# Performance work log

Measured on AMD Instinct MI355X. Metric: run time of the kernel, lower is better.

The kernel has to match this reference:

```python
import jax, jax.numpy as jnp
import numpy as np
from jax import lax

B, N, S, K, C, OUT = 8, 4096, 1024, 24, 64, 128
IN = 2 * C + 3  # 131: grouped(C+3) concat anchor feature(C)
EPS_BN = 1e-5


def _bn_params(key, c):
    k1, k2, k3, k4 = jax.random.split(key, 4)
    gamma = jax.random.uniform(k1, (c,), minval=0.5, maxval=1.5)
    beta = jax.random.normal(k2, (c,)) * 0.1
    mean = jax.random.normal(k3, (c,)) * 0.1
    var = jax.random.uniform(k4, (c,), minval=0.5, maxval=1.5)
    return jnp.stack([gamma, beta, mean, var])  # [4,c]


def setup_inputs() -> dict:
    key = jax.random.key(0)
    ks = jax.random.split(key, 20)
    w = lambda k, shp: jax.random.normal(k, shp) * 0.05
    inp = {
        "xyz": jax.random.normal(ks[0], (B, N, 3)),
        "points": jax.random.normal(ks[1], (B, N, C)),
        "affine_alpha": jnp.ones((1, 1, 1, C + 3)),
        "affine_beta": jnp.zeros((1, 1, 1, C + 3)),
        "transfer_w": w(ks[2], (OUT, IN)),
        "transfer_b": jnp.zeros((OUT,)),
        "transfer_bn": _bn_params(ks[3], OUT),
        "pre_w1": w(ks[4], (2, OUT, OUT)),
        "pre_b1": jnp.zeros((2, OUT)),
        "pre_bn1": jnp.stack([_bn_params(ks[5], OUT), _bn_params(ks[6], OUT)]),
        "pre_w2": w(ks[7], (2, OUT, OUT)),
        "pre_b2": jnp.zeros((2, OUT)),
        "pre_bn2": jnp.stack([_bn_params(ks[8], OUT), _bn_params(ks[9], OUT)]),
        "pos_w1": w(ks[10], (2, OUT, OUT)),
        "pos_b1": jnp.zeros((2, OUT)),
        "pos_bn1": jnp.stack([_bn_params(ks[11], OUT), _bn_params(ks[12], OUT)]),
        "pos_w2": w(ks[13], (2, OUT, OUT)),
        "pos_b2": jnp.zeros((2, OUT)),
        "pos_bn2": jnp.stack([_bn_params(ks[14], OUT), _bn_params(ks[15], OUT)]),
    }
    return inp


def _gather(x, idx):
    # x: [B,N,D], idx: [B,...] -> [B,...,D]
    return jax.vmap(lambda a, i: a[i])(x, idx)


def _sqdist(a, b):
    # a: [B,S,3], b: [B,N,3] -> [B,S,N]
    return (jnp.sum(a * a, -1)[:, :, None] + jnp.sum(b * b, -1)[:, None, :]
            - 2.0 * jnp.einsum('bsd,bnd->bsn', a, b))


def _fps(xyz, s):
    # furthest point sampling, starts at index 0 (matches CUDA pointnet2 impl)
    b, n, _ = xyz.shape
    def step(carry, _):
        dist, last = carry
        p = jnp.take_along_axis(xyz, last[:, None, None], axis=1)  # [B,1,3]
        d = jnp.sum((xyz - p) ** 2, -1)
        dist = jnp.minimum(dist, d)
        nxt = jnp.argmax(dist, axis=-1).astype(jnp.int32)
        return (dist, nxt), nxt
    init = (jnp.full((b, n), 1e10, xyz.dtype), jnp.zeros((b,), jnp.int32))
    _, idxs = lax.scan(step, init, None, length=s - 1)  # [S-1,B]
    return jnp.concatenate([jnp.zeros((1, b), jnp.int32), idxs], 0).T  # [B,S]


def _conv_bn(x, w, b, bn, act=True):
    # 1x1 Conv1d + BatchNorm (eval mode) + optional ReLU. x: [M,Cin,L]
    y = jnp.einsum('oc,mcl->mol', w, x) + b[None, :, None]
    g, be, mu, var = bn[0], bn[1], bn[2], bn[3]
    y = (y - mu[None, :, None]) * (g[None, :, None] / jnp.sqrt(var[None, :, None] + EPS_BN)) + be[None, :, None]
    return jax.nn.relu(y) if act else y


def _res_block(x, w1, b1, bn1, w2, b2, bn2):
    y = _conv_bn(x, w1, b1, bn1, act=True)
    y = _conv_bn(y, w2, b2, bn2, act=False)
    return jax.nn.relu(y + x)


def reference(xyz, points, affine_alpha, affine_beta,
              transfer_w, transfer_b, transfer_bn,
              pre_w1, pre_b1, pre_bn1, pre_w2, pre_b2, pre_bn2,
              pos_w1, pos_b1, pos_bn1, pos_w2, pos_b2, pos_bn2):
    b, n, _ = xyz.shape
    # ---- LocalGrouper ----
    fps_idx = _fps(xyz, S)                      # [B,S]
    new_xyz = _gather(xyz, fps_idx)             # [B,S,3]
    new_points = _gather(points, fps_idx)       # [B,S,C]
    d = _sqdist(new_xyz, xyz)                   # [B,S,N]
    _, idx = lax.top_k(-d, K)                   # k nearest -> [B,S,K]
    grouped_xyz = _gather(xyz, idx)             # [B,S,K,3]
    grouped_points = _gather(points, idx)       # [B,S,K,C]
    grouped = jnp.concatenate([grouped_points, grouped_xyz], -1)  # [B,S,K,C+3]
    # anchor normalize
    mean = jnp.concatenate([new_points, new_xyz], -1)[:, :, None, :]
    diff = grouped - mean
    std = jnp.std(diff.reshape(b, -1), axis=-1, ddof=1)[:, None, None, None]
    grouped = affine_alpha * (diff / (std + 1e-5)) + affine_beta
    anchor = jnp.broadcast_to(new_points[:, :, None, :], (b, S, K, C))
    feats = jnp.concatenate([grouped, anchor], -1)  # [B,S,K,2C+3]
    # ---- PreExtraction ----
    x = feats.transpose(0, 1, 3, 2).reshape(b * S, IN, K)  # [B*S,131,K]
    x = _conv_bn(x, transfer_w, transfer_b, transfer_bn, act=True)
    for i in range(2):
        x = _res_block(x, pre_w1[i], pre_b1[i], pre_bn1[i], pre_w2[i], pre_b2[i], pre_bn2[i])
    x = jnp.max(x, axis=-1)                     # adaptive max pool over K
    x = x.reshape(b, S, OUT).transpose(0, 2, 1)  # [B,OUT,S]
    # ---- PosExtraction ----
    for i in range(2):
        x = _res_block(x, pos_w1[i], pos_b1[i], pos_bn1[i], pos_w2[i], pos_b2[i], pos_bn2[i])
    return x  # [B,128,1024]
```

## Files before the change

### kernel.cpp

```cpp
#include <hip/hip_runtime.h>
#include <hip/hip_bf16.h>
#include <stdint.h>
#include <math.h>

#define DEVINL static __device__ __forceinline__

static constexpr int BB = 8, NN = 4096, SS = 1024, KK = 24, CC = 64;
static constexpr int INCH = 131, OUTCH = 128;

typedef __attribute__((ext_vector_type(8))) short short8v;
typedef __attribute__((ext_vector_type(4))) float f32x4;
typedef __attribute__((ext_vector_type(2))) float f32x2;

#define MFMA16(a, b, c) __builtin_amdgcn_mfma_f32_16x16x32_bf16(a, b, c, 0, 0, 0)

DEVINL unsigned short bfhi(float v) {
  return (unsigned short)(__float_as_uint(v) >> 16);
}
DEVINL float bfhif(float v) {
  return __uint_as_float(__float_as_uint(v) & 0xFFFF0000u);
}
DEVINL unsigned short bflo(float v) {
  float r = __fsub_rn(v, bfhif(v));
  return (unsigned short)(__float_as_uint(r) >> 16);
}

__global__ __launch_bounds__(256) void k_prep_xyz(
    const float* __restrict__ xyz,
    float* __restrict__ xs, float* __restrict__ ys,
    float* __restrict__ zs, float* __restrict__ sb) {
  int e = blockIdx.x * 256 + threadIdx.x;
  if (e >= BB * NN) return;
  float x = xyz[e * 3 + 0];
  float y = xyz[e * 3 + 1];
  float z = xyz[e * 3 + 2];
  xs[e] = x; ys[e] = y; zs[e] = z;
  sb[e] = __fadd_rn(__fadd_rn(__fmul_rn(x, x), __fmul_rn(y, y)), __fmul_rn(z, z));
}

__global__ __launch_bounds__(256) void k_prep_w(
    const float* __restrict__ tw,
    const float* __restrict__ pw1, const float* __restrict__ pw2,
    const float* __restrict__ qw1, const float* __restrict__ qw2,
    const float* __restrict__ tb,  const float* __restrict__ tbn,
    const float* __restrict__ pb1, const float* __restrict__ pbn1,
    const float* __restrict__ pb2, const float* __restrict__ pbn2,
    const float* __restrict__ qb1, const float* __restrict__ qbn1,
    const float* __restrict__ qb2, const float* __restrict__ qbn2,
    float* __restrict__ wt_sq, float* __restrict__ bnsb,
    unsigned short* __restrict__ wfhi, unsigned short* __restrict__ wflo) {
  int e = blockIdx.x * 256 + threadIdx.x;
  const int NSQ = 8 * 128 * 128;
  const int NBN = 9 * 128;
  const int NFR = 168 * 64;
  if (e < NSQ) {
    int layer = e >> 14, m = e & 16383;
    int ci = m >> 7, co = m & 127;
    const float* src;
    switch (layer) {
      case 0: src = pw1;         break;
      case 1: src = pw2;         break;
      case 2: src = pw1 + 16384; break;
      case 3: src = pw2 + 16384; break;
      case 4: src = qw1;         break;
      case 5: src = qw2;         break;
      case 6: src = qw1 + 16384; break;
      default: src = qw2 + 16384; break;
    }
    wt_sq[layer * 16384 + ci * 128 + co] = src[co * 128 + ci];
  } else if (e < NSQ + NBN) {
    int r = e - NSQ;
    int L = r >> 7, co = r & 127;
    const float *bn, *bc;
    switch (L) {
      case 0: bn = tbn;        bc = tb;        break;
      case 1: bn = pbn1;       bc = pb1;       break;
      case 2: bn = pbn2;       bc = pb2;       break;
      case 3: bn = pbn1 + 512; bc = pb1 + 128; break;
      case 4: bn = pbn2 + 512; bc = pb2 + 128; break;
      case 5: bn = qbn1;       bc = qb1;       break;
      case 6: bn = qbn2;       bc = qb2;       break;
      case 7: bn = qbn1 + 512; bc = qb1 + 128; break;
      default: bn = qbn2 + 512; bc = qb2 + 128; break;
    }
    float g  = bn[co];
    float be = bn[128 + co];
    float mu = bn[256 + co];
    float va = bn[384 + co];
    float bcv = bc[co];
    float sc = g / sqrtf(va + 1e-5f);
    float bi = (bcv - mu) * sc + be;
    bnsb[L * 256 + co] = sc;
    bnsb[L * 256 + 128 + co] = bi;
  } else if (e < NSQ + NBN + NFR) {
    int r = e - (NSQ + NBN);
    int T = r >> 6, lane = r & 63;
    int L, ks, mt;
    if (T < 40) { L = 0; ks = T >> 3; mt = T & 7; }
    else { int r2 = T - 40; L = 1 + (r2 >> 5); int r3 = r2 & 31; ks = r3 >> 3; mt = r3 & 7; }
    const float* src;
    int K, stride;
    switch (L) {
      case 0:  src = tw;          K = 131; stride = 131; break;
      case 1:  src = pw1;         K = 128; stride = 128; break;
      case 2:  src = pw2;         K = 128; stride = 128; break;
      case 3:  src = pw1 + 16384; K = 128; stride = 128; break;
      default: src = pw2 + 16384; K = 128; stride = 128; break;
    }
    int m = lane & 15, kb = lane >> 4;
    int co = mt * 16 + m;
    int base = (T * 64 + lane) * 8;
#pragma unroll
    for (int j = 0; j < 8; j++) {
      int ci = ks * 32 + kb * 8 + j;
      float w = (ci < K) ? src[co * stride + ci] : 0.f;
      wfhi[base + j] = bfhi(w);
      wflo[base + j] = bflo(w);
    }
  }
}

DEVINL float wave_max_f32_l63(float x) {
#define STEPF(C)                                                                \
  {                                                                             \
    int o = __builtin_amdgcn_update_dpp(0xff800000, __float_as_int(x), C, 0xf, 0xf, false); \
    x = fmaxf(x, __int_as_float(o));                                            \
  }
  STEPF(0x111) STEPF(0x112) STEPF(0x114) STEPF(0x118) STEPF(0x142) STEPF(0x143)
#undef STEPF
  return x;
}

__global__ __launch_bounds__(256, 1) void k_fps(
    const float* __restrict__ xs, const float* __restrict__ ys,
    const float* __restrict__ zs, const float* __restrict__ sb,
    const float* __restrict__ points,
    float* __restrict__ nxyz, float* __restrict__ sa, float* __restrict__ newp) {
  __shared__ float lxl[NN], lyl[NN], lzl[NN];
  __shared__ unsigned long long pk[2][4];
  __shared__ int fpsl[SS];
  const int b = blockIdx.x, t = threadIdx.x;
  const int wid = t >> 6, lane = t & 63;
  const float* bx = xs + b * NN;
  const float* by = ys + b * NN;
  const float* bz = zs + b * NN;
  f32x2 rx[8], ry[8], rz[8], d[8];
  const int n0 = t * 16;
#pragma unroll
  for (int j = 0; j < 8; j++) {
    int n = n0 + 2 * j;
    rx[j].x = bx[n]; rx[j].y = bx[n + 1];
    ry[j].x = by[n]; ry[j].y = by[n + 1];
    rz[j].x = bz[n]; rz[j].y = bz[n + 1];
    lxl[n] = rx[j].x; lxl[n + 1] = rx[j].y;
    lyl[n] = ry[j].x; lyl[n + 1] = ry[j].y;
    lzl[n] = rz[j].x; lzl[n + 1] = rz[j].y;
    d[j].x = 1e10f; d[j].y = 1e10f;
  }
  __syncthreads();
  float px = lxl[0], py = lyl[0], pz = lzl[0];
  if (t == 0) fpsl[0] = 0;
#pragma unroll 1
  for (int i = 1; i < SS; i++) {
    float bestval = -1.f;
    int bestn = 0;
    f32x2 px2, py2, pz2;
    px2.x = px; px2.y = px;
    py2.x = py; py2.y = py;
    pz2.x = pz; pz2.y = pz;
#pragma unroll
    for (int j = 0; j < 8; j++) {
      f32x2 dd;
      {
#pragma clang fp contract(off)
        f32x2 dx = rx[j] - px2;
        f32x2 dy = ry[j] - py2;
        f32x2 dz = rz[j] - pz2;
        dd = (dx * dx + dy * dy) + dz * dz;
      }
      float nd0 = fminf(d[j].x, dd.x);
      float nd1 = fminf(d[j].y, dd.y);
      d[j].x = nd0; d[j].y = nd1;
      if (nd0 > bestval) { bestval = nd0; bestn = n0 + 2 * j; }
      if (nd1 > bestval) { bestval = nd1; bestn = n0 + 2 * j + 1; }
    }
    float wmax = __int_as_float(
        __builtin_amdgcn_readlane(__float_as_int(wave_max_f32_l63(bestval)), 63));
    unsigned long long el = __ballot(bestval == wmax);
    int fl = (int)__ffsll(el) - 1;
    int wn = __builtin_amdgcn_readlane(bestn, fl);
    if (lane == 0)
      pk[i & 1][wid] = ((unsigned long long)__float_as_uint(wmax) << 32) |
                       (unsigned)(NN - 1 - wn);
    __syncthreads();
    const unsigned long long* P = pk[i & 1];
    unsigned long long k0 = P[0], k1 = P[1], k2 = P[2], k3 = P[3];
    unsigned long long m01 = k1 > k0 ? k1 : k0;
    unsigned long long m23 = k3 > k2 ? k3 : k2;
    unsigned long long g = m23 > m01 ? m23 : m01;
    int n = NN - 1 - (int)(unsigned)g;
    px = lxl[n]; py = lyl[n]; pz = lzl[n];
    if (t == 0) fpsl[i] = n;
  }
  __syncthreads();
  for (int s = t; s < SS; s += 256) {
    int row = fpsl[s];
    nxyz[(b * SS + s) * 3 + 0] = lxl[row];
    nxyz[(b * SS + s) * 3 + 1] = lyl[row];
    nxyz[(b * SS + s) * 3 + 2] = lzl[row];
    sa[b * SS + s] = sb[b * NN + row];
  }
  for (int e = t; e < SS * CC; e += 256) {
    int s = e >> 6, c = e & 63;
    int row = fpsl[s];
    newp[(b * SS + s) * CC + c] = points[(b * NN + row) * CC + c];
  }
}

__global__ __launch_bounds__(256, 2) void k_knn(
    const float* __restrict__ xs, const float* __restrict__ ys,
    const float* __restrict__ zs,
    const float* __restrict__ nxyz, const float* __restrict__ sa,
    const float* __restrict__ points, const float* __restrict__ newp,
    int* __restrict__ knn, double* __restrict__ spart) {
  __shared__ float lx[NN], ly[NN], lz[NN];
  __shared__ int selk[4][KK];
  const int blk = blockIdx.x, t = threadIdx.x, wid = t >> 6, lane = t & 63;
  const int b = blk >> 8;
  for (int e = t; e < NN; e += 256) {
    lx[e] = xs[b * NN + e]; ly[e] = ys[b * NN + e]; lz[e] = zs[b * NN + e];
  }
  __syncthreads();
  const int q = blk * 4 + wid;
  float qx = nxyz[q * 3 + 0], qy = nxyz[q * 3 + 1], qz = nxyz[q * 3 + 2];
  float qa = sa[q];
  unsigned keys[64];
#pragma unroll
  for (int j = 0; j < 64; j++) {
    int n = j * 64 + lane;
    float x = lx[n], y = ly[n], z = lz[n];
    float sbn = __fadd_rn(__fadd_rn(__fmul_rn(x, x), __fmul_rn(y, y)), __fmul_rn(z, z));
    float dot = __fadd_rn(__fadd_rn(__fmul_rn(qx, x), __fmul_rn(qy, y)), __fmul_rn(qz, z));
    float dd = __fsub_rn(__fadd_rn(qa, sbn), __fmul_rn(2.0f, dot));
    unsigned u = __float_as_uint(dd);
    u ^= (0x80000000u | (unsigned)((int)u >> 31));
    keys[j] = u;
  }
#pragma unroll 1
  for (int r = 0; r < KK; r++) {
    unsigned bv = keys[0];
    int bj = 0;
#pragma unroll
    for (int j = 1; j < 64; j++) {
      if (keys[j] < bv) { bv = keys[j]; bj = j; }
    }
    unsigned long long gk = ((unsigned long long)bv << 32) | (unsigned)(bj * 64 + lane);
#pragma unroll
    for (int m = 1; m < 64; m <<= 1) {
      unsigned long long o = __shfl_xor(gk, m);
      gk = o < gk ? o : gk;
    }
    int n = (int)(unsigned)gk;
    if (lane == 0) { knn[q * KK + r] = n; selk[wid][r] = n; }
    if (lane == (n & 63)) {
      int jj = n >> 6;
#pragma unroll
      for (int j = 0; j < 64; j++)
        if (j == jj) keys[j] = 0xFFFFFFFFu;
    }
  }
  double s1 = 0.0, s2 = 0.0;
#pragma unroll 1
  for (int i = 0; i < 26; i++) {
    int e = lane + 64 * i;
    if (e < KK * 67) {
      int k = e / 67, c = e - k * 67;
      int n = selk[wid][k];
      float g, mm;
      if (c < CC) {
        g = points[(b * NN + n) * CC + c];
        mm = newp[q * CC + c];
      } else {
        int cc = c - CC;
        g = cc == 0 ? lx[n] : (cc == 1 ? ly[n] : lz[n]);
        mm = nxyz[q * 3 + cc];
      }
      float v = __fsub_rn(g, mm);
      s1 += (double)v;
      s2 += (double)v * (double)v;
    }
  }
#pragma unroll
  for (int m = 1; m < 64; m <<= 1) {
    s1 += __shfl_xor(s1, m);
    s2 += __shfl_xor(s2, m);
  }
  if (lane == 0) { spart[q * 2 + 0] = s1; spart[q * 2 + 1] = s2; }
}

__global__ __launch_bounds__(256) void k_stdfin(
    const double* __restrict__ spart, float* __restrict__ stdp) {
  __shared__ double a1[256], a2[256];
  const int b = blockIdx.x, t = threadIdx.x;
  double s1 = 0.0, s2 = 0.0;
  for (int i = t; i < SS; i += 256) {
    s1 += spart[(b * SS + i) * 2 + 0];
    s2 += spart[(b * SS + i) * 2 + 1];
  }
  a1[t] = s1; a2[t] = s2;
  __syncthreads();
  for (int w = 128; w > 0; w >>= 1) {
    if (t < w) { a1[t] += a1[t + w]; a2[t] += a2[t + w]; }
    __syncthreads();
  }
  if (t == 0) {
    const double n = (double)SS * KK * 67;
    double m = a1[0] / n;
    double var = (a2[0] - a1[0] * m) / (n - 1.0);
    if (var < 0.0) var = 0.0;
    float stdf = (float)sqrt(var);
    stdp[b] = stdf + 1e-5f;
  }
}

static constexpr int BST = 168;
static constexpr int XST = 132;

__global__ __launch_bounds__(256, 4) void k_pre(
    const float* __restrict__ points,
    const float* __restrict__ alpha, const float* __restrict__ beta,
    const float* __restrict__ xs, const float* __restrict__ ys, const float* __restrict__ zs,
    const float* __restrict__ nxyz, const float* __restrict__ newp,
    const float* __restrict__ stdp, const int* __restrict__ knn,
    const unsigned short* __restrict__ wfhi, const unsigned short* __restrict__ wflo,
    const float* __restrict__ bnsb, float* __restrict__ pre_out) {
  __shared__ unsigned short Bhi[32 * BST];
  __shared__ unsigned short Blo[32 * BST];
  __shared__ float Xres[32 * XST];
  __shared__ int kn[KK];
  __shared__ float npl[CC], nxl[3], al[67], bt[67];
  __shared__ float stds;
  const int q = blockIdx.x, b = q >> 10, t = threadIdx.x;
  for (int e = t; e < 32 * BST; e += 256) { Bhi[e] = 0; Blo[e] = 0; }
  if (t < KK) kn[t] = knn[q * KK + t];
  if (t < 67) { al[t] = alpha[t]; bt[t] = beta[t]; }
  if (t < CC) npl[t] = newp[q * CC + t];
  if (t < 3) nxl[t] = nxyz[q * 3 + t];
  if (t == 0) stds = stdp[b];
  __syncthreads();
  for (int e = t; e < KK * 67; e += 256) {
    int k = e / 67, c = e - k * 67;
    int n = kn[k];
    float g, mm;
    if (c < CC) {
      g = points[(b * NN + n) * CC + c];
      mm = npl[c];
    } else {
      int cc = c - CC;
      g = cc == 0 ? xs[b * NN + n] : (cc == 1 ? ys[b * NN + n] : zs[b * NN + n]);
      mm = nxl[cc];
    }
    float v = __fsub_rn(g, mm);
    float tt = __fdiv_rn(v, stds);
    float val = __fadd_rn(__fmul_rn(al[c], tt), bt[c]);
    Bhi[k * BST + c] = bfhi(val);
    Blo[k * BST + c] = bflo(val);
  }
  for (int e = t; e < CC * KK; e += 256) {
    int c = e / KK, k = e - c * KK;
    float val = npl[c];
    Bhi[k * BST + 67 + c] = bfhi(val);
    Blo[k * BST + 67 + c] = bflo(val);
  }
  __syncthreads();

  const int wv = t >> 6, lane = t & 63;
  const int g4 = lane >> 4;
  const int l15 = lane & 15;
  const int mt0 = wv * 2;

#pragma unroll
  for (int L = 0; L < 5; ++L) {
    const int nks = (L == 0) ? 5 : 4;
    const int wtb = (L == 0) ? 0 : (8 + 32 * L);
    const bool addres = (L == 2) || (L == 4);
    const bool wres = (L == 0) || (L == 2);
    const bool pool = (L == 4);
    f32x4 acc00 = {0.f, 0.f, 0.f, 0.f}, acc01 = {0.f, 0.f, 0.f, 0.f};
    f32x4 acc10 = {0.f, 0.f, 0.f, 0.f}, acc11 = {0.f, 0.f, 0.f, 0.f};
#pragma unroll
    for (int ks = 0; ks < nks; ++ks) {
      const int tb = (wtb + ks * 8 + mt0) * 64 + lane;
      short8v wh0 = *(const short8v*)(wfhi + tb * 8);
      short8v wh1 = *(const short8v*)(wfhi + (tb + 64) * 8);
      short8v wl0 = *(const short8v*)(wflo + tb * 8);
      short8v wl1 = *(const short8v*)(wflo + (tb + 64) * 8);
      const int bo = l15 * BST + ks * 32 + g4 * 8;
      short8v bh0 = *(const short8v*)&Bhi[bo];
      short8v bh1 = *(const short8v*)&Bhi[bo + 16 * BST];
      short8v bl0 = *(const short8v*)&Blo[bo];
      short8v bl1 = *(const short8v*)&Blo[bo + 16 * BST];
      acc00 = MFMA16(wh0, bh0, acc00);
      acc00 = MFMA16(wl0, bh0, acc00);
      acc00 = MFMA16(wh0, bl0, acc00);
      acc01 = MFMA16(wh0, bh1, acc01);
      acc01 = MFMA16(wl0, bh1, acc01);
      acc01 = MFMA16(wh0, bl1, acc01);
      acc10 = MFMA16(wh1, bh0, acc10);
      acc10 = MFMA16(wl1, bh0, acc10);
      acc10 = MFMA16(wh1, bl0, acc10);
      acc11 = MFMA16(wh1, bh1, acc11);
      acc11 = MFMA16(wl1, bh1, acc11);
      acc11 = MFMA16(wh1, bl1, acc11);
    }
    __syncthreads();
    float mx0[4] = {0.f, 0.f, 0.f, 0.f};
    float mx1[4] = {0.f, 0.f, 0.f, 0.f};
    auto ep = [&](const f32x4& a, int mt_i, int nt, float* mxr) {
      const int co0 = (mt0 + mt_i) * 16 + g4 * 4;
      const int kp = nt * 16 + l15;
      const bool valid = kp < KK;
      f32x4 scv = *(const f32x4*)(bnsb + L * 256 + co0);
      f32x4 biv = *(const f32x4*)(bnsb + L * 256 + 128 + co0);
      float y[4];
#pragma unroll
      for (int r = 0; r < 4; r++) y[r] = fmaf(a[r], scv[r], biv[r]);
      if (addres && valid) {
        f32x4 xr = *(const f32x4*)&Xres[kp * XST + co0];
#pragma unroll
        for (int r = 0; r < 4; r++) y[r] += xr[r];
      }
#pragma unroll
      for (int r = 0; r < 4; r++) y[r] = fmaxf(y[r], 0.f);
      if (wres && valid) {
        f32x4 o = {y[0], y[1], y[2], y[3]};
        *(f32x4*)&Xres[kp * XST + co0] = o;
      }
      if (!pool) {
        if (valid) {
          unsigned b0 = __float_as_uint(y[0]), b1 = __float_as_uint(y[1]);
          unsigned b2 = __float_as_uint(y[2]), b3 = __float_as_uint(y[3]);
          unsigned h01 = (b0 >> 16) | (b1 & 0xFFFF0000u);
          unsigned h23 = (b2 >> 16) | (b3 & 0xFFFF0000u);
          *(uint2*)&Bhi[kp * BST + co0] = make_uint2(h01, h23);
          float r0 = __fsub_rn(y[0], __uint_as_float(b0 & 0xFFFF0000u));
          float r1 = __fsub_rn(y[1], __uint_as_float(b1 & 0xFFFF0000u));
          float r2 = __fsub_rn(y[2], __uint_as_float(b2 & 0xFFFF0000u));
          float r3 = __fsub_rn(y[3], __uint_as_float(b3 & 0xFFFF0000u));
          unsigned l01 = (__float_as_uint(r0) >> 16) | (__float_as_uint(r1) & 0xFFFF0000u);
          unsigned l23 = (__float_as_uint(r2) >> 16) | (__float_as_uint(r3) & 0xFFFF0000u);
          *(uint2*)&Blo[kp * BST + co0] = make_uint2(l01, l23);
        }
      } else {
#pragma unroll
        for (int r = 0; r < 4; r++) {
          float v = valid ? y[r] : 0.f;
          mxr[r] = fmaxf(mxr[r], v);
        }
      }
    };
    ep(acc00, 0, 0, mx0);
    ep(acc01, 0, 1, mx0);
    ep(acc10, 1, 0, mx1);
    ep(acc11, 1, 1, mx1);
    if (!pool) {
      __syncthreads();
    } else {
#pragma unroll
      for (int dstep = 1; dstep < 16; dstep <<= 1) {
#pragma unroll
        for (int r = 0; r < 4; r++) {
          mx0[r] = fmaxf(mx0[r], __shfl_xor(mx0[r], dstep));
          mx1[r] = fmaxf(mx1[r], __shfl_xor(mx1[r], dstep));
        }
      }
      if (l15 == 0) {
        f32x4 o0 = {mx0[0], mx0[1], mx0[2], mx0[3]};
        f32x4 o1 = {mx1[0], mx1[1], mx1[2], mx1[3]};
        *(f32x4*)&pre_out[q * 128 + mt0 * 16 + g4 * 4] = o0;
        *(f32x4*)&pre_out[q * 128 + (mt0 + 1) * 16 + g4 * 4] = o1;
      }
    }
  }
}

__global__ __launch_bounds__(256, 2) void k_pos(
    const float* __restrict__ pre_out, const float* __restrict__ wt_sq,
    const float* __restrict__ bnsb, float* __restrict__ out) {
  __shared__ float X[128][68];
  __shared__ float Y[128][68];
  const int blk = blockIdx.x, t = threadIdx.x;
  const int b = blk >> 4, s0 = (blk & 15) << 6;
  for (int e = t; e < 128 * 64; e += 256) {
    int sl = e >> 7, c = e & 127;
    X[c][sl] = pre_out[(b * SS + s0 + sl) * 128 + c];
  }
  __syncthreads();
  const int co0 = (t >> 3) << 2, p0 = (t & 7) << 3;
  float acc[4][8];
  auto conv = [&](const float (*IN)[68], const float* wt) {
#pragma unroll
    for (int i = 0; i < 4; i++)
#pragma unroll
      for (int j = 0; j < 8; j++) acc[i][j] = 0.f;
#pragma unroll 2
    for (int ci = 0; ci < 128; ci++) {
      float4 w = *(const float4*)(wt + ci * 128 + co0);
      float4 r0 = *(const float4*)&IN[ci][p0];
      float4 r1 = *(const float4*)&IN[ci][p0 + 4];
      float a[8] = {r0.x, r0.y, r0.z, r0.w, r1.x, r1.y, r1.z, r1.w};
#pragma unroll
      for (int j = 0; j < 8; j++) {
        acc[0][j] = fmaf(w.x, a[j], acc[0][j]);
        acc[1][j] = fmaf(w.y, a[j], acc[1][j]);
        acc[2][j] = fmaf(w.z, a[j], acc[2][j]);
        acc[3][j] = fmaf(w.w, a[j], acc[3][j]);
      }
    }
  };
  conv(X, wt_sq + 4 * 16384);
  {
    const float* bn = bnsb + 5 * 256;
#pragma unroll
    for (int i = 0; i < 4; i++) {
      float sc = bn[co0 + i], bi = bn[128 + co0 + i];
#pragma unroll
      for (int j = 0; j < 8; j++)
        Y[co0 + i][p0 + j] = fmaxf(fmaf(acc[i][j], sc, bi), 0.f);
    }
  }
  __syncthreads();
  conv(Y, wt_sq + 5 * 16384);
  {
    const float* bn = bnsb + 6 * 256;
#pragma unroll
    for (int i = 0; i < 4; i++) {
      float sc = bn[co0 + i], bi = bn[128 + co0 + i];
#pragma unroll
      for (int j = 0; j < 8; j++)
        X[co0 + i][p0 + j] =
            fmaxf(fmaf(acc[i][j], sc, bi) + X[co0 + i][p0 + j], 0.f);
    }
  }
  __syncthreads();
  conv(X, wt_sq + 6 * 16384);
  {
    const float* bn = bnsb + 7 * 256;
#pragma unroll
    for (int i = 0; i < 4; i++) {
      float sc = bn[co0 + i], bi = bn[128 + co0 + i];
#pragma unroll
      for (int j = 0; j < 8; j++)
        Y[co0 + i][p0 + j] = fmaxf(fmaf(acc[i][j], sc, bi), 0.f);
    }
  }
  __syncthreads();
  conv(Y, wt_sq + 7 * 16384);
  {
    const float* bn = bnsb + 8 * 256;
#pragma unroll
    for (int i = 0; i < 4; i++) {
      float sc = bn[co0 + i], bi = bn[128 + co0 + i];
      float4 o0, o1;
      float v;
      v = fmaxf(fmaf(acc[i][0], sc, bi) + X[co0 + i][p0 + 0], 0.f); o0.x = v;
      v = fmaxf(fmaf(acc[i][1], sc, bi) + X[co0 + i][p0 + 1], 0.f); o0.y = v;
      v = fmaxf(fmaf(acc[i][2], sc, bi) + X[co0 + i][p0 + 2], 0.f); o0.z = v;
      v = fmaxf(fmaf(acc[i][3], sc, bi) + X[co0 + i][p0 + 3], 0.f); o0.w = v;
      v = fmaxf(fmaf(acc[i][4], sc, bi) + X[co0 + i][p0 + 4], 0.f); o1.x = v;
      v = fmaxf(fmaf(acc[i][5], sc, bi) + X[co0 + i][p0 + 5], 0.f); o1.y = v;
      v = fmaxf(fmaf(acc[i][6], sc, bi) + X[co0 + i][p0 + 6], 0.f); o1.z = v;
      v = fmaxf(fmaf(acc[i][7], sc, bi) + X[co0 + i][p0 + 7], 0.f); o1.w = v;
      float* op = &out[(size_t)(b * 128 + co0 + i) * SS + s0 + p0];
      *(float4*)op = o0;
      *(float4*)(op + 4) = o1;
    }
  }
}

extern "C" void kernel_launch(void* const* d_in, const int* in_sizes, int n_in,
                              void* d_out, int out_size, void* d_ws, size_t ws_size,
                              hipStream_t stream) {
  (void)in_sizes; (void)n_in; (void)out_size; (void)ws_size;
  const float* xyz    = (const float*)d_in[0];
  const float* points = (const float*)d_in[1];
  const float* alpha  = (const float*)d_in[2];
  const float* beta   = (const float*)d_in[3];
  const float* tw     = (const float*)d_in[4];
  const float* tb     = (const float*)d_in[5];
  const float* tbn    = (const float*)d_in[6];
  const float* pw1    = (const float*)d_in[7];
  const float* pb1    = (const float*)d_in[8];
  const float* pbn1   = (const float*)d_in[9];
  const float* pw2    = (const float*)d_in[10];
  const float* pb2    = (const float*)d_in[11];
  const float* pbn2   = (const float*)d_in[12];
  const float* qw1    = (const float*)d_in[13];
  const float* qb1    = (const float*)d_in[14];
  const float* qbn1   = (const float*)d_in[15];
  const float* qw2    = (const float*)d_in[16];
  const float* qb2    = (const float*)d_in[17];
  const float* qbn2   = (const float*)d_in[18];

  char* ws = (char*)d_ws;
  size_t off = 0;
  auto alloc = [&](size_t bytes) -> char* {
    char* p = ws + off;
    off += (bytes + 255) & ~(size_t)255;
    return p;
  };
  float*  xs    = (float*)alloc(BB * NN * 4);
  float*  ys    = (float*)alloc(BB * NN * 4);
  float*  zs    = (float*)alloc(BB * NN * 4);
  float*  sb    = (float*)alloc(BB * NN * 4);
  float*  wt_sq = (float*)alloc(8 * 16384 * 4);
  float*  bnsb  = (float*)alloc(9 * 256 * 4);
  unsigned short* wfhi = (unsigned short*)alloc(168 * 512 * 2);
  unsigned short* wflo = (unsigned short*)alloc(168 * 512 * 2);
  float*  nxyz  = (float*)alloc(BB * SS * 3 * 4);
  float*  sa    = (float*)alloc(BB * SS * 4);
  float*  newp  = (float*)alloc(BB * SS * CC * 4);
  int*    knn   = (int*)alloc(BB * SS * KK * 4);
  double* spart = (double*)alloc(BB * SS * 2 * 8);
  float*  stdp  = (float*)alloc(256);
  float*  preo  = (float*)alloc((size_t)BB * SS * 128 * 4);
  float*  out   = (float*)d_out;

  const int prep_n = 8 * 128 * 128 + 9 * 128 + 168 * 64;
  hipLaunchKernelGGL(k_prep_xyz, dim3((BB * NN + 255) / 256), dim3(256), 0, stream,
                     xyz, xs, ys, zs, sb);
  hipLaunchKernelGGL(k_prep_w, dim3((prep_n + 255) / 256), dim3(256), 0, stream,
                     tw, pw1, pw2, qw1, qw2, tb, tbn, pb1, pbn1, pb2, pbn2,
                     qb1, qbn1, qb2, qbn2, wt_sq, bnsb, wfhi, wflo);
  hipLaunchKernelGGL(k_fps, dim3(BB), dim3(256), 0, stream,
                     xs, ys, zs, sb, points, nxyz, sa, newp);
  hipLaunchKernelGGL(k_knn, dim3(BB * SS / 4), dim3(256), 0, stream,
                     xs, ys, zs, nxyz, sa, points, newp, knn, spart);
  hipLaunchKernelGGL(k_stdfin, dim3(BB), dim3(256), 0, stream, spart, stdp);
  hipLaunchKernelGGL(k_pre, dim3(BB * SS), dim3(256), 0, stream,
                     points, alpha, beta, xs, ys, zs, nxyz, newp, stdp, knn,
                     wfhi, wflo, bnsb, preo);
  hipLaunchKernelGGL(k_pos, dim3(BB * SS / 64), dim3(256), 0, stream,
                     preo, wt_sq, bnsb, out);
}
```

Measured before the change: 1.036 ms.

## Process two query groups per k_pre block and use DPP wave-min in kNN

k_pre now handles two sampled centroids per block, so each block keeps two sets of shared-memory activation tiles and reuses every loaded weight fragment for both groups' MFMAs. This halves global weight traffic per centroid and halves the block count. The cost is twice the LDS footprint, more accumulator registers and lower launch bounds occupancy (4 to 2). Separately, the kNN argmin over a wave replaces a 64-bit shuffle-xor butterfly with two 32-bit DPP min reductions plus readlane.

```diff
diff --git a/kernel.cpp b/kernel.cpp
--- a/kernel.cpp
+++ b/kernel.cpp
@@ -131,6 +131,28 @@
   return x;
 }
 
+DEVINL unsigned wave_min_u32_l63(unsigned x) {
+#define STEPU(C)                                                                \
+  {                                                                             \
+    unsigned o = (unsigned)__builtin_amdgcn_update_dpp(-1, (int)x, C, 0xf, 0xf, false); \
+    x = o < x ? o : x;                                                          \
+  }
+  STEPU(0x111) STEPU(0x112) STEPU(0x114) STEPU(0x118) STEPU(0x142) STEPU(0x143)
+#undef STEPU
+  return x;
+}
+
+DEVINL int wave_min_i32_l63(int x) {
+#define STEPI(C)                                                                \
+  {                                                                             \
+    int o = __builtin_amdgcn_update_dpp(0x7fffffff, x, C, 0xf, 0xf, false);     \
+    x = o < x ? o : x;                                                          \
+  }
+  STEPI(0x111) STEPI(0x112) STEPI(0x114) STEPI(0x118) STEPI(0x142) STEPI(0x143)
+#undef STEPI
+  return x;
+}
+
 __global__ __launch_bounds__(256, 1) void k_fps(
     const float* __restrict__ xs, const float* __restrict__ ys,
     const float* __restrict__ zs, const float* __restrict__ sb,
@@ -254,13 +276,10 @@
     for (int j = 1; j < 64; j++) {
       if (keys[j] < bv) { bv = keys[j]; bj = j; }
     }
-    unsigned long long gk = ((unsigned long long)bv << 32) | (unsigned)(bj * 64 + lane);
-#pragma unroll
-    for (int m = 1; m < 64; m <<= 1) {
-      unsigned long long o = __shfl_xor(gk, m);
-      gk = o < gk ? o : gk;
-    }
-    int n = (int)(unsigned)gk;
+    unsigned wmin = (unsigned)__builtin_amdgcn_readlane(
+        (int)wave_min_u32_l63(bv), 63);
+    int en = (bv == wmin) ? (bj * 64 + lane) : 0x7FFFFFFF;
+    int n = __builtin_amdgcn_readlane(wave_min_i32_l63(en), 63);
     if (lane == 0) { knn[q * KK + r] = n; selk[wid][r] = n; }
     if (lane == (n & 63)) {
       int jj = n >> 6;
@@ -326,7 +345,7 @@
 static constexpr int BST = 168;
 static constexpr int XST = 132;
 
-__global__ __launch_bounds__(256, 4) void k_pre(
+__global__ __launch_bounds__(256, 2) void k_pre(
     const float* __restrict__ points,
     const float* __restrict__ alpha, const float* __restrict__ beta,
     const float* __restrict__ xs, const float* __restrict__ ys, const float* __restrict__ zs,
@@ -334,43 +353,49 @@
     const float* __restrict__ stdp, const int* __restrict__ knn,
     const unsigned short* __restrict__ wfhi, const unsigned short* __restrict__ wflo,
     const float* __restrict__ bnsb, float* __restrict__ pre_out) {
-  __shared__ unsigned short Bhi[32 * BST];
-  __shared__ unsigned short Blo[32 * BST];
-  __shared__ float Xres[32 * XST];
-  __shared__ int kn[KK];
-  __shared__ float npl[CC], nxl[3], al[67], bt[67];
+  __shared__ unsigned short Bhi[2][32 * BST];
+  __shared__ unsigned short Blo[2][32 * BST];
+  __shared__ float Xres[2][32 * XST];
+  __shared__ int kn[2][KK];
+  __shared__ float npl[2][CC], nxl[2][3], al[67], bt[67];
   __shared__ float stds;
-  const int q = blockIdx.x, b = q >> 10, t = threadIdx.x;
-  for (int e = t; e < 32 * BST; e += 256) { Bhi[e] = 0; Blo[e] = 0; }
-  if (t < KK) kn[t] = knn[q * KK + t];
+  const int q0 = blockIdx.x * 2, b = q0 >> 10, t = threadIdx.x;
+  for (int e = t; e < 32 * BST; e += 256) {
+    Bhi[0][e] = 0; Blo[0][e] = 0; Bhi[1][e] = 0; Blo[1][e] = 0;
+  }
+  if (t < 2 * KK) kn[t / KK][t % KK] = knn[(q0 + t / KK) * KK + (t % KK)];
   if (t < 67) { al[t] = alpha[t]; bt[t] = beta[t]; }
-  if (t < CC) npl[t] = newp[q * CC + t];
-  if (t < 3) nxl[t] = nxyz[q * 3 + t];
+  if (t < 2 * CC) { int s = t >> 6, c = t & 63; npl[s][c] = newp[(q0 + s) * CC + c]; }
+  if (t < 6) { int s = t / 3, c = t % 3; nxl[s][c] = nxyz[(q0 + s) * 3 + c]; }
   if (t == 0) stds = stdp[b];
   __syncthreads();
-  for (int e = t; e < KK * 67; e += 256) {
-    int k = e / 67, c = e - k * 67;
-    int n = kn[k];
+  for (int e = t; e < 2 * KK * 67; e += 256) {
+    int s = e / (KK * 67);
+    int r = e - s * (KK * 67);
+    int k = r / 67, c = r - k * 67;
+    int n = kn[s][k];
     float g, mm;
     if (c < CC) {
       g = points[(b * NN + n) * CC + c];
-      mm = npl[c];
+      mm = npl[s][c];
     } else {
       int cc = c - CC;
       g = cc == 0 ? xs[b * NN + n] : (cc == 1 ? ys[b * NN + n] : zs[b * NN + n]);
-      mm = nxl[cc];
+      mm = nxl[s][cc];
     }
     float v = __fsub_rn(g, mm);
     float tt = __fdiv_rn(v, stds);
     float val = __fadd_rn(__fmul_rn(al[c], tt), bt[c]);
-    Bhi[k * BST + c] = bfhi(val);
-    Blo[k * BST + c] = bflo(val);
-  }
-  for (int e = t; e < CC * KK; e += 256) {
-    int c = e / KK, k = e - c * KK;
-    float val = npl[c];
-    Bhi[k * BST + 67 + c] = bfhi(val);
-    Blo[k * BST + 67 + c] = bflo(val);
+    Bhi[s][k * BST + c] = bfhi(val);
+    Blo[s][k * BST + c] = bflo(val);
+  }
+  for (int e = t; e < 2 * CC * KK; e += 256) {
+    int s = e / (CC * KK);
+    int r = e - s * (CC * KK);
+    int c = r / KK, k = r - c * KK;
+    float val = npl[s][c];
+    Bhi[s][k * BST + 67 + c] = bfhi(val);
+    Blo[s][k * BST + 67 + c] = bflo(val);
   }
   __syncthreads();
 
@@ -386,8 +411,8 @@
     const bool addres = (L == 2) || (L == 4);
     const bool wres = (L == 0) || (L == 2);
     const bool pool = (L == 4);
-    f32x4 acc00 = {0.f, 0.f, 0.f, 0.f}, acc01 = {0.f, 0.f, 0.f, 0.f};
-    f32x4 acc10 = {0.f, 0.f, 0.f, 0.f}, acc11 = {0.f, 0.f, 0.f, 0.f};
+    f32x4 aA00 = {0,0,0,0}, aA01 = {0,0,0,0}, aA10 = {0,0,0,0}, aA11 = {0,0,0,0};
+    f32x4 aB00 = {0,0,0,0}, aB01 = {0,0,0,0}, aB10 = {0,0,0,0}, aB11 = {0,0,0,0};
 #pragma unroll
     for (int ks = 0; ks < nks; ++ks) {
       const int tb = (wtb + ks * 8 + mt0) * 64 + lane;
@@ -396,27 +421,47 @@
       short8v wl0 = *(const short8v*)(wflo + tb * 8);
       short8v wl1 = *(const short8v*)(wflo + (tb + 64) * 8);
       const int bo = l15 * BST + ks * 32 + g4 * 8;
-      short8v bh0 = *(const short8v*)&Bhi[bo];
-      short8v bh1 = *(const short8v*)&Bhi[bo + 16 * BST];
-      short8v bl0 = *(const short8v*)&Blo[bo];
-      short8v bl1 = *(const short8v*)&Blo[bo + 16 * BST];
-      acc00 = MFMA16(wh0, bh0, acc00);
-      acc00 = MFMA16(wl0, bh0, acc00);
-      acc00 = MFMA16(wh0, bl0, acc00);
-      acc01 = MFMA16(wh0, bh1, acc01);
-      acc01 = MFMA16(wl0, bh1, acc01);
-      acc01 = MFMA16(wh0, bl1, acc01);
-      acc10 = MFMA16(wh1, bh0, acc10);
-      acc10 = MFMA16(wl1, bh0, acc10);
-      acc10 = MFMA16(wh1, bl0, acc10);
-      acc11 = MFMA16(wh1, bh1, acc11);
-      acc11 = MFMA16(wl1, bh1, acc11);
-      acc11 = MFMA16(wh1, bl1, acc11);
+      {
+        short8v bh0 = *(const short8v*)&Bhi[0][bo];
+        short8v bh1 = *(const short8v*)&Bhi[0][bo + 16 * BST];
+        short8v bl0 = *(const short8v*)&Blo[0][bo];
+        short8v bl1 = *(const short8v*)&Blo[0][bo + 16 * BST];
+        aA00 = MFMA16(wh0, bh0, aA00);
+        aA00 = MFMA16(wl0, bh0, aA00);
+        aA00 = MFMA16(wh0, bl0, aA00);
+        aA01 = MFMA16(wh0, bh1, aA01);
+        aA01 = MFMA16(wl0, bh1, aA01);
+        aA01 = MFMA16(wh0, bl1, aA01);
+        aA10 = MFMA16(wh1, bh0, aA10);
+        aA10 = MFMA16(wl1, bh0, aA10);
+        aA10 = MFMA16(wh1, bl0, aA10);
+        aA11 = MFMA16(wh1, bh1, aA11);
+        aA11 = MFMA16(wl1, bh1, aA11);
+        aA11 = MFMA16(wh1, bl1, aA11);
+      }
+      {
+        short8v bh0 = *(const short8v*)&Bhi[1][bo];
+        short8v bh1 = *(const short8v*)&Bhi[1][bo + 16 * BST];
+        short8v bl0 = *(const short8v*)&Blo[1][bo];
+        short8v bl1 = *(const short8v*)&Blo[1][bo + 16 * BST];
+        aB00 = MFMA16(wh0, bh0, aB00);
+        aB00 = MFMA16(wl0, bh0, aB00);
+        aB00 = MFMA16(wh0, bl0, aB00);
+        aB01 = MFMA16(wh0, bh1, aB01);
+        aB01 = MFMA16(wl0, bh1, aB01);
+        aB01 = MFMA16(wh0, bl1, aB01);
+        aB10 = MFMA16(wh1, bh0, aB10);
+        aB10 = MFMA16(wl1, bh0, aB10);
+        aB10 = MFMA16(wh1, bl0, aB10);
+        aB11 = MFMA16(wh1, bh1, aB11);
+        aB11 = MFMA16(wl1, bh1, aB11);
+        aB11 = MFMA16(wh1, bl1, aB11);
+      }
     }
     __syncthreads();
-    float mx0[4] = {0.f, 0.f, 0.f, 0.f};
-    float mx1[4] = {0.f, 0.f, 0.f, 0.f};
-    auto ep = [&](const f32x4& a, int mt_i, int nt, float* mxr) {
+    float mxA0[4] = {0,0,0,0}, mxA1[4] = {0,0,0,0};
+    float mxB0[4] = {0,0,0,0}, mxB1[4] = {0,0,0,0};
+    auto ep = [&](const f32x4& a, int s, int mt_i, int nt, float* mxr) {
       const int co0 = (mt0 + mt_i) * 16 + g4 * 4;
       const int kp = nt * 16 + l15;
       const bool valid = kp < KK;
@@ -426,7 +471,7 @@
 #pragma unroll
       for (int r = 0; r < 4; r++) y[r] = fmaf(a[r], scv[r], biv[r]);
       if (addres && valid) {
-        f32x4 xr = *(const f32x4*)&Xres[kp * XST + co0];
+        f32x4 xr = *(const f32x4*)&Xres[s][kp * XST + co0];
 #pragma unroll
         for (int r = 0; r < 4; r++) y[r] += xr[r];
       }
@@ -434,7 +479,7 @@
       for (int r = 0; r < 4; r++) y[r] = fmaxf(y[r], 0.f);
       if (wres && valid) {
         f32x4 o = {y[0], y[1], y[2], y[3]};
-        *(f32x4*)&Xres[kp * XST + co0] = o;
+        *(f32x4*)&Xres[s][kp * XST + co0] = o;
       }
       if (!pool) {
         if (valid) {
@@ -442,14 +487,14 @@
           unsigned b2 = __float_as_uint(y[2]), b3 = __float_as_uint(y[3]);
           unsigned h01 = (b0 >> 16) | (b1 & 0xFFFF0000u);
           unsigned h23 = (b2 >> 16) | (b3 & 0xFFFF0000u);
-          *(uint2*)&Bhi[kp * BST + co0] = make_uint2(h01, h23);
+          *(uint2*)&Bhi[s][kp * BST + co0] = make_uint2(h01, h23);
           float r0 = __fsub_rn(y[0], __uint_as_float(b0 & 0xFFFF0000u));
           float r1 = __fsub_rn(y[1], __uint_as_float(b1 & 0xFFFF0000u));
           float r2 = __fsub_rn(y[2], __uint_as_float(b2 & 0xFFFF0000u));
           float r3 = __fsub_rn(y[3], __uint_as_float(b3 & 0xFFFF0000u));
           unsigned l01 = (__float_as_uint(r0) >> 16) | (__float_as_uint(r1) & 0xFFFF0000u);
           unsigned l23 = (__float_as_uint(r2) >> 16) | (__float_as_uint(r3) & 0xFFFF0000u);
-          *(uint2*)&Blo[kp * BST + co0] = make_uint2(l01, l23);
+          *(uint2*)&Blo[s][kp * BST + co0] = make_uint2(l01, l23);
         }
       } else {
 #pragma unroll
@@ -459,10 +504,14 @@
         }
       }
     };
-    ep(acc00, 0, 0, mx0);
-    ep(acc01, 0, 1, mx0);
-    ep(acc10, 1, 0, mx1);
-    ep(acc11, 1, 1, mx1);
+    ep(aA00, 0, 0, 0, mxA0);
+    ep(aA01, 0, 0, 1, mxA0);
+    ep(aA10, 0, 1, 0, mxA1);
+    ep(aA11, 0, 1, 1, mxA1);
+    ep(aB00, 1, 0, 0, mxB0);
+    ep(aB01, 1, 0, 1, mxB0);
+    ep(aB10, 1, 1, 0, mxB1);
+    ep(aB11, 1, 1, 1, mxB1);
     if (!pool) {
       __syncthreads();
     } else {
@@ -470,15 +519,21 @@
       for (int dstep = 1; dstep < 16; dstep <<= 1) {
 #pragma unroll
         for (int r = 0; r < 4; r++) {
-          mx0[r] = fmaxf(mx0[r], __shfl_xor(mx0[r], dstep));
-          mx1[r] = fmaxf(mx1[r], __shfl_xor(mx1[r], dstep));
+          mxA0[r] = fmaxf(mxA0[r], __shfl_xor(mxA0[r], dstep));
+          mxA1[r] = fmaxf(mxA1[r], __shfl_xor(mxA1[r], dstep));
+          mxB0[r] = fmaxf(mxB0[r], __shfl_xor(mxB0[r], dstep));
+          mxB1[r] = fmaxf(mxB1[r], __shfl_xor(mxB1[r], dstep));
         }
       }
       if (l15 == 0) {
-        f32x4 o0 = {mx0[0], mx0[1], mx0[2], mx0[3]};
-        f32x4 o1 = {mx1[0], mx1[1], mx1[2], mx1[3]};
-        *(f32x4*)&pre_out[q * 128 + mt0 * 16 + g4 * 4] = o0;
-        *(f32x4*)&pre_out[q * 128 + (mt0 + 1) * 16 + g4 * 4] = o1;
+        f32x4 oA0 = {mxA0[0], mxA0[1], mxA0[2], mxA0[3]};
+        f32x4 oA1 = {mxA1[0], mxA1[1], mxA1[2], mxA1[3]};
+        f32x4 oB0 = {mxB0[0], mxB0[1], mxB0[2], mxB0[3]};
+        f32x4 oB1 = {mxB1[0], mxB1[1], mxB1[2], mxB1[3]};
+        *(f32x4*)&pre_out[q0 * 128 + mt0 * 16 + g4 * 4] = oA0;
+        *(f32x4*)&pre_out[q0 * 128 + (mt0 + 1) * 16 + g4 * 4] = oA1;
+        *(f32x4*)&pre_out[(q0 + 1) * 128 + mt0 * 16 + g4 * 4] = oB0;
+        *(f32x4*)&pre_out[(q0 + 1) * 128 + (mt0 + 1) * 16 + g4 * 4] = oB1;
       }
     }
   }
@@ -637,7 +692,7 @@
   hipLaunchKernelGGL(k_knn, dim3(BB * SS / 4), dim3(256), 0, stream,
                      xs, ys, zs, nxyz, sa, points, newp, knn, spart);
   hipLaunchKernelGGL(k_stdfin, dim3(BB), dim3(256), 0, stream, spart, stdp);
-  hipLaunchKernelGGL(k_pre, dim3(BB * SS), dim3(256), 0, stream,
+  hipLaunchKernelGGL(k_pre, dim3(BB * SS / 2), dim3(256), 0, stream,
                      points, alpha, beta, xs, ys, zs, nxyz, newp, stdp, knn,
                      wfhi, wflo, bnsb, preo);
   hipLaunchKernelGGL(k_pos, dim3(BB * SS / 64), dim3(256), 0, stream,
```

Result: slower. 1.098 ms (+6.0%).
